# Kernel optimization log

Hardware: AMD Instinct MI355X
Metric: run time of the kernel (lower is better)

## Reference

```python
import jax, jax.numpy as jnp
import numpy as np

B, S, HID = 2, 2048, 1024
H, D = 16, 64
R = 128  # max_relative_position
NREL = 2 * R + 1


def _make_indices():
    i = np.arange(S)[:, None]
    j = np.arange(S)[None, :]
    return np.clip(j - i + R, 0, 2 * R).astype(np.int32)  # [S, S]


def setup_inputs() -> dict:
    key = jax.random.key(0)
    ks = jax.random.split(key, 10)
    sc = 0.02
    return {
        "hidden_states": jax.random.normal(ks[0], (B, S, HID), jnp.float32),
        "st_mask": jnp.ones((B, S), jnp.float32),
        "Wq": jax.random.normal(ks[1], (HID, HID), jnp.float32) * sc,
        "bq": jnp.zeros((HID,), jnp.float32),
        "Wk": jax.random.normal(ks[2], (HID, HID), jnp.float32) * sc,
        "bk": jnp.zeros((HID,), jnp.float32),
        "Wv": jax.random.normal(ks[3], (HID, HID), jnp.float32) * sc,
        "bv": jnp.zeros((HID,), jnp.float32),
        "rel_key_emb": jax.random.normal(ks[4], (NREL, D), jnp.float32) * sc,
        "rel_val_emb": jax.random.normal(ks[5], (NREL, D), jnp.float32) * sc,
        "indices": jnp.asarray(_make_indices()),
    }


def reference(hidden_states, st_mask, Wq, bq, Wk, bk, Wv, bv, rel_key_emb, rel_val_emb, indices):
    b, s, _ = hidden_states.shape

    def heads(x):  # [B,S,HID] -> [B,H,S,D]
        return x.reshape(b, s, H, D).transpose(0, 2, 1, 3)

    q = heads(hidden_states @ Wq.T + bq)
    k = heads(hidden_states @ Wk.T + bk)
    v = heads(hidden_states @ Wv.T + bv)

    scores = jnp.einsum("bhqd,bhkd->bhqk", q, k) / jnp.sqrt(jnp.asarray(D, q.dtype))

    # relative position key bias: gather per (query, key) pair
    rel_scores = jnp.einsum("bhqd,rd->bhqr", q, rel_key_emb)  # [B,H,S,NREL]
    idx = indices[None, None]  # [1,1,S,S]
    scores = scores + jnp.take_along_axis(rel_scores, jnp.broadcast_to(idx, scores.shape), axis=3)

    mask = (1.0 - st_mask) * -10000.0  # [B,S]
    scores = scores + mask[:, None, None, :]

    probs = jax.nn.softmax(scores, axis=-1)  # dropout is identity at eval
    context = jnp.einsum("bhqk,bhkd->bhqd", probs, v)

    # scatter-add probs back onto relative buckets for the value path
    qi = jnp.arange(s)[:, None]  # [S,1] broadcasts with indices [S,S]
    rel_probs = jnp.zeros((b, H, s, NREL), probs.dtype).at[:, :, qi, indices].add(probs)
    context = context + jnp.einsum("bhqr,rd->bhqd", rel_probs, rel_val_emb)

    return context.transpose(0, 2, 1, 3).reshape(b, s, H * D)
```

## Files before the change

### kernel.cpp

```cpp
#include <hip/hip_runtime.h>
#include <math.h>

typedef __bf16 bf16;
typedef __bf16 bf16x8 __attribute__((ext_vector_type(8)));
typedef __bf16 bf16x4 __attribute__((ext_vector_type(4)));
typedef float  f32x4  __attribute__((ext_vector_type(4)));

namespace {
constexpr int B_ = 2, S_ = 2048, HID_ = 1024, H_ = 16, D_ = 64, R_ = 128, NREL_ = 257;
constexpr float LOG2E_ = 1.44269504f;
constexpr float QSC_ = 0.125f * LOG2E_;
}

static __device__ __forceinline__ f32x4 mfma16(bf16x8 a, bf16x8 b, f32x4 c) {
  return __builtin_amdgcn_mfma_f32_16x16x32_bf16(a, b, c, 0, 0, 0);
}
static __device__ __forceinline__ void split2(float f, bf16 &hi, bf16 &lo) {
  hi = (bf16)f; lo = (bf16)(f - (float)hi);
}
static __device__ __forceinline__ float fexp2(float x) {
  return __builtin_amdgcn_exp2f(x);
}
static __device__ __forceinline__ void gload16(const bf16* g, bf16* l) {
  __builtin_amdgcn_global_load_lds(
      (const __attribute__((address_space(1))) void*)g,
      (__attribute__((address_space(3))) void*)l, 16, 0, 0);
}

__global__ __launch_bounds__(256) void prep_kernel(
    const float* __restrict__ st_mask, const float* __restrict__ rkE,
    const float* __restrict__ rvE, const float* __restrict__ hidden,
    const float* __restrict__ Wq, const float* __restrict__ Wk,
    const float* __restrict__ Wv,
    float* __restrict__ msk2, bf16* __restrict__ rkEb, bf16* __restrict__ rvTb,
    bf16* __restrict__ Ahg, bf16* __restrict__ Alg, bf16* __restrict__ Wbg)
{
  const int t0 = blockIdx.x * 256 + threadIdx.x;
  const int NT = gridDim.x * 256;
  for (int t = t0; t < B_ * S_; t += NT)
    msk2[t] = (1.f - st_mask[t]) * -10000.f * LOG2E_;
  for (int t = t0; t < 272 * 64; t += NT) {
    const int bk = t >> 6, d = t & 63;
    rkEb[t] = (bk < NREL_) ? (bf16)(rkE[bk * D_ + d] * 8.0f) : (bf16)0.f;
  }
  for (int t = t0; t < 64 * 288; t += NT) {
    const int d = t / 288, c = t - d * 288;
    rvTb[t] = (c < NREL_) ? (bf16)rvE[c * D_ + d] : (bf16)0.f;
  }
  for (int t = t0; t < (B_ * S_ * HID_) / 4; t += NT) {
    const float4 a = ((const float4*)hidden)[t];
    const float av[4] = {a.x, a.y, a.z, a.w};
    bf16x4 h, o;
#pragma unroll
    for (int i = 0; i < 4; ++i) {
      bf16 th, tl;
      split2(av[i], th, tl);
      h[i] = th; o[i] = tl;
    }
    *(bf16x4*)&Ahg[t * 4] = h;
    *(bf16x4*)&Alg[t * 4] = o;
  }
  for (int t = t0; t < 3 * (HID_ * HID_) / 4; t += NT) {
    const int s = t >> 18, i = t & 262143;
    const float4 wv4 = ((const float4*)(s == 0 ? Wq : s == 1 ? Wk : Wv))[i];
    bf16x4 h;
    h[0] = (bf16)wv4.x; h[1] = (bf16)wv4.y; h[2] = (bf16)wv4.z; h[3] = (bf16)wv4.w;
    *(bf16x4*)&Wbg[s * 1048576 + i * 4] = h;
  }
}

__global__ __launch_bounds__(256, 2) void qkv_mfma_kernel(
    const bf16* __restrict__ Ahg, const bf16* __restrict__ Alg,
    const bf16* __restrict__ Wbg,
    const float* __restrict__ bq, const float* __restrict__ bk,
    const float* __restrict__ bv,
    bf16* __restrict__ Qh, bf16* __restrict__ Ql,
    bf16* __restrict__ Kb, bf16* __restrict__ Vt)
{
  const int swz = ((int)blockIdx.x & 7) * 64 + ((int)blockIdx.x >> 3);
  const int m0 = (swz >> 4) * 128;
  const int n0 = (swz & 15) * 64;
  const int tid = threadIdx.x;
  const int l = tid & 63, w = tid >> 6;
  const int cl = l & 15, g = l >> 4;

  __shared__ __align__(16) bf16 AhS[2][4096];
  __shared__ __align__(16) bf16 AlS[2][4096];
  __shared__ __align__(16) bf16 WS[2][3][2048];

  const int r0 = tid >> 2;
  const int csw = (((tid & 3) ^ (r0 & 3)) << 3);
  const size_t aoff0 = (size_t)(m0 + r0) * HID_ + csw;
  const size_t aoff1 = (size_t)(m0 + 64 + r0) * HID_ + csw;
  const size_t woff  = (size_t)(n0 + r0) * HID_ + csw;
  const int wb = w * 512;

  const int rA0 = w * 16 + cl;
  const int eA0 = rA0 * 32 + 8 * (g ^ (rA0 & 3));
  const int eA1 = eA0 + 2048;
  const int eW  = cl * 32 + 8 * (g ^ (cl & 3));

  f32x4 acc[2][3][4];
#pragma unroll
  for (int hf = 0; hf < 2; ++hf)
#pragma unroll
    for (int s = 0; s < 3; ++s)
#pragma unroll
      for (int nf = 0; nf < 4; ++nf)
#pragma unroll
        for (int i = 0; i < 4; ++i) acc[hf][s][nf][i] = 0.f;

  gload16(Ahg + aoff0, &AhS[0][wb]);
  gload16(Ahg + aoff1, &AhS[0][2048 + wb]);
  gload16(Alg + aoff0, &AlS[0][wb]);
  gload16(Alg + aoff1, &AlS[0][2048 + wb]);
  gload16(Wbg + woff,           &WS[0][0][wb]);
  gload16(Wbg + 1048576 + woff, &WS[0][1][wb]);
  gload16(Wbg + 2097152 + woff, &WS[0][2][wb]);
  __syncthreads();

  int cur = 0;
  for (int kt = 0; kt < HID_ / 32; ++kt) {
    if (kt + 1 < HID_ / 32) {
      const size_t ko = (size_t)(kt + 1) * 32;
      bf16* ah = &AhS[cur ^ 1][0]; bf16* al = &AlS[cur ^ 1][0];
      gload16(Ahg + aoff0 + ko, ah + wb);
      gload16(Ahg + aoff1 + ko, ah + 2048 + wb);
      gload16(Alg + aoff0 + ko, al + wb);
      gload16(Alg + aoff1 + ko, al + 2048 + wb);
      gload16(Wbg + woff + ko,           &WS[cur ^ 1][0][wb]);
      gload16(Wbg + 1048576 + woff + ko, &WS[cur ^ 1][1][wb]);
      gload16(Wbg + 2097152 + woff + ko, &WS[cur ^ 1][2][wb]);
    }

    const bf16x8 fah0 = *(const bf16x8*)&AhS[cur][eA0];
    const bf16x8 fah1 = *(const bf16x8*)&AhS[cur][eA1];
    const bf16x8 fal0 = *(const bf16x8*)&AlS[cur][eA0];
    const bf16x8 fal1 = *(const bf16x8*)&AlS[cur][eA1];
#pragma unroll
    for (int s = 0; s < 3; ++s)
#pragma unroll
      for (int nf = 0; nf < 4; ++nf) {
        const bf16x8 fb = *(const bf16x8*)&WS[cur][s][nf * 512 + eW];
        acc[0][s][nf] = mfma16(fah0, fb, acc[0][s][nf]);
        acc[0][s][nf] = mfma16(fal0, fb, acc[0][s][nf]);
        acc[1][s][nf] = mfma16(fah1, fb, acc[1][s][nf]);
        acc[1][s][nf] = mfma16(fal1, fb, acc[1][s][nf]);
      }
    __syncthreads();
    cur ^= 1;
  }

  const float* bs_[3] = {bq, bk, bv};
#pragma unroll
  for (int s = 0; s < 3; ++s)
#pragma unroll
    for (int nf = 0; nf < 4; ++nf) {
      const int n = n0 + nf * 16 + cl;
      const float bias = bs_[s][n];
      const int hd = n >> 6, d = n & 63;
#pragma unroll
      for (int hf = 0; hf < 2; ++hf)
#pragma unroll
        for (int reg = 0; reg < 4; ++reg) {
          const int m = m0 + hf * 64 + w * 16 + g * 4 + reg;
          const int b = m >> 11, sq = m & (S_ - 1);
          const float val = acc[hf][s][nf][reg] + bias;
          if (s == 0) {
            bf16 h, o; split2(val * QSC_, h, o);
            const size_t idx = ((size_t)(b * H_ + hd) * S_ + sq) * D_ + d;
            Qh[idx] = h; Ql[idx] = o;
          } else if (s == 1) {
            Kb[((size_t)(b * H_ + hd) * S_ + sq) * D_ + d] = (bf16)val;
          } else {
            const int jo = sq & 63;
            const int mc = (jo & 32) | (((jo >> 3) & 1) << 4) | (((jo >> 2) & 1) << 3)
                         | (((jo >> 4) & 1) << 2) | (jo & 3);
            Vt[(((size_t)(b * H_ + hd) * (S_ / 64) + (sq >> 6)) * D_ + d) * 64 + mc]
                = (bf16)val;
          }
        }
    }
}

__global__ __launch_bounds__(512, 4) void attn_kernel(
    const bf16* __restrict__ Qh, const bf16* __restrict__ Ql,
    const bf16* __restrict__ Kb, const bf16* __restrict__ Vt,
    const float* __restrict__ msk2, const bf16* __restrict__ rkEb,
    const bf16* __restrict__ rvTb, float* __restrict__ out)
{
  const int swz = ((int)blockIdx.x & 7) * 128 + ((int)blockIdx.x >> 3);
  const int qt = swz & 31, h = (swz >> 5) & 15, b = swz >> 9;
  const int q0 = qt * 64;
  const int tid = threadIdx.x;
  const int l = tid & 63, w = tid >> 6;
  const int wq = (w & 3) * 16;
  const int wh = w >> 2;
  const int cl = l & 15, g = l >> 4, kg8 = g * 8;
  const int lq = wq + cl;

  __shared__ __align__(16) unsigned char U[36864];
  __shared__ __align__(16) bf16 T[64][288];
  __shared__ float red[2][3][64];
  __shared__ float lsum_s[64];

  bf16* kb0 = (bf16*)&U[0];
  bf16* kb1 = (bf16*)&U[8192];
  bf16* vb0 = (bf16*)&U[16384];
  bf16* vb1 = (bf16*)&U[24576];
  float* ctxredf = (float*)&U[0];

  const size_t bh = (size_t)(b * H_ + h) * S_;
  const bf16* Kbase = Kb + bh * D_;
  const bf16* Vbase = Vt + bh * D_;
  const float* mbase = msk2 + b * S_;

  const int tKr = tid >> 3;
  const int koff = tKr * 64 + (((tid & 7) ^ (tKr & 7)) << 3);

  gload16(Kbase + koff, kb0 + w * 512);
  gload16(Vbase + koff, vb0 + w * 512);

  bf16x8 qh0, qh1, ql0, ql1;
  {
    const size_t base = (bh + q0 + lq) * D_ + kg8;
    qh0 = *(const bf16x8*)(Qh + base);
    qh1 = *(const bf16x8*)(Qh + base + 32);
    ql0 = *(const bf16x8*)(Ql + base);
    ql1 = *(const bf16x8*)(Ql + base + 32);
  }

  {
    const int nt0 = wh ? 9 : 0, ntE = wh ? 17 : 9;
    for (int nt = nt0; nt < ntE; ++nt) {
      f32x4 r; r[0] = r[1] = r[2] = r[3] = 0.f;
      const bf16x8 a0 = *(const bf16x8*)(rkEb + (size_t)(nt * 16 + cl) * 64 + kg8);
      const bf16x8 a1 = *(const bf16x8*)(rkEb + (size_t)(nt * 16 + cl) * 64 + 32 + kg8);
      r = mfma16(a0, qh0, r); r = mfma16(a0, ql0, r);
      r = mfma16(a1, qh1, r); r = mfma16(a1, ql1, r);
      bf16x4 pk;
#pragma unroll
      for (int reg = 0; reg < 4; ++reg) pk[reg] = (bf16)r[reg];
      *(bf16x4*)&T[lq][nt * 16 + g * 4] = pk;
    }
  }
  __syncthreads();

  const float rs_lo = (float)T[lq][0];
  const float rs_hi = (float)T[lq][2 * R_];
  const int qg = q0 + lq;

  f32x4 ctx[4];
#pragma unroll
  for (int nf = 0; nf < 4; ++nf) { ctx[nf][0]=0.f; ctx[nf][1]=0.f; ctx[nf][2]=0.f; ctx[nf][3]=0.f; }
  float lsum = 0.f, plo = 0.f, phi = 0.f;

  const int r00 = wh * 32 + cl, r10 = wh * 32 + 16 + cl;
  const int e00 = r00 * 64 + 8 * (g ^ (r00 & 7)), e01 = r00 * 64 + 8 * ((4 + g) ^ (r00 & 7));
  const int e10 = r10 * 64 + 8 * (g ^ (r10 & 7)), e11 = r10 * 64 + 8 * ((4 + g) ^ (r10 & 7));
  int fv0, fv1, fv2, fv3;
  {
    const int rd0 = 0 * 16 + cl, rd1 = 1 * 16 + cl, rd2 = 2 * 16 + cl, rd3 = 3 * 16 + cl;
    fv0 = rd0 * 64 + 8 * ((4 * wh + g) ^ (rd0 & 7));
    fv1 = rd1 * 64 + 8 * ((4 * wh + g) ^ (rd1 & 7));
    fv2 = rd2 * 64 + 8 * ((4 * wh + g) ^ (rd2 & 7));
    fv3 = rd3 * 64 + 8 * ((4 * wh + g) ^ (rd3 & 7));
  }

  int cur = 0;
  for (int kt = 0; kt < S_ / 64; ++kt) {
    if (kt + 1 < S_ / 64) {
      gload16(Kbase + (size_t)(kt + 1) * 4096 + koff, (cur ? kb0 : kb1) + w * 512);
      gload16(Vbase + (size_t)(kt + 1) * 4096 + koff, (cur ? vb0 : vb1) + w * 512);
    }

    const bf16* kc = cur ? kb1 : kb0;
    const bf16x8 a00 = *(const bf16x8*)&kc[e00];
    const bf16x8 a01 = *(const bf16x8*)&kc[e01];
    const bf16x8 a10 = *(const bf16x8*)&kc[e10];
    const bf16x8 a11 = *(const bf16x8*)&kc[e11];

    f32x4 s0, s1;
    s0[0]=s0[1]=s0[2]=s0[3]=0.f; s1[0]=s1[1]=s1[2]=s1[3]=0.f;
    __builtin_amdgcn_s_setprio(1);
    s0 = mfma16(a00, qh0, s0); s0 = mfma16(a00, ql0, s0);
    s0 = mfma16(a01, qh1, s0); s0 = mfma16(a01, ql1, s0);
    s1 = mfma16(a10, qh0, s1); s1 = mfma16(a10, ql0, s1);
    s1 = mfma16(a11, qh1, s1); s1 = mfma16(a11, ql1, s1);
    __builtin_amdgcn_s_setprio(0);

    const int j0 = kt * 64 + wh * 32;
    const float4 mk0 = *(const float4*)(mbase + j0 + g * 4);
    const float4 mk1 = *(const float4*)(mbase + j0 + 16 + g * 4);
    const int dlt = kt * 64 - q0;
    const int mode = (dlt <= -192) ? 0 : (dlt >= 192 ? 1 : 2);

    bf16x4 pk0, pk1;
#pragma unroll
    for (int nf = 0; nf < 2; ++nf) {
      const f32x4 sa = nf ? s1 : s0;
      const float4 mkv = nf ? mk1 : mk0;
      const float mks[4] = {mkv.x, mkv.y, mkv.z, mkv.w};
      float p[4];
      if (mode == 0) {
#pragma unroll
        for (int reg = 0; reg < 4; ++reg) p[reg] = fexp2(sa[reg] + rs_lo + mks[reg]);
        plo += (p[0] + p[1]) + (p[2] + p[3]);
      } else if (mode == 1) {
#pragma unroll
        for (int reg = 0; reg < 4; ++reg) p[reg] = fexp2(sa[reg] + rs_hi + mks[reg]);
        phi += (p[0] + p[1]) + (p[2] + p[3]);
      } else {
        const int jb = j0 + nf * 16 + g * 4;
#pragma unroll
        for (int reg = 0; reg < 4; ++reg) {
          const int bkv = jb + reg - qg + R_;
          const int bkc = bkv < 0 ? 0 : (bkv > 2 * R_ ? 2 * R_ : bkv);
          const float pv = fexp2(sa[reg] + (float)T[lq][bkc] + mks[reg]);
          p[reg] = pv;
          if (bkv <= 0)           plo += pv;
          else if (bkv >= 2 * R_) phi += pv;
          else                    T[lq][bkv] = (bf16)pv;
        }
      }
      lsum += (p[0] + p[1]) + (p[2] + p[3]);
      bf16x4 pk;
#pragma unroll
      for (int reg = 0; reg < 4; ++reg) pk[reg] = (bf16)p[reg];
      if (nf == 0) pk0 = pk; else pk1 = pk;
    }

    const bf16x8 pa = __builtin_shufflevector(pk0, pk1, 0, 1, 2, 3, 4, 5, 6, 7);
    const bf16* vc = cur ? vb1 : vb0;
    __builtin_amdgcn_s_setprio(1);
    ctx[0] = mfma16(pa, *(const bf16x8*)&vc[fv0], ctx[0]);
    ctx[1] = mfma16(pa, *(const bf16x8*)&vc[fv1], ctx[1]);
    ctx[2] = mfma16(pa, *(const bf16x8*)&vc[fv2], ctx[2]);
    ctx[3] = mfma16(pa, *(const bf16x8*)&vc[fv3], ctx[3]);
    __builtin_amdgcn_s_setprio(0);
    __syncthreads();
    cur ^= 1;
  }

  lsum += __shfl_xor(lsum, 16); lsum += __shfl_xor(lsum, 32);
  plo  += __shfl_xor(plo, 16);  plo  += __shfl_xor(plo, 32);
  phi  += __shfl_xor(phi, 16);  phi  += __shfl_xor(phi, 32);
  if (l < 16) {
    red[wh][0][wq + l] = lsum;
    red[wh][1][wq + l] = plo;
    red[wh][2][wq + l] = phi;
  }
  __syncthreads();

  {
    const int nfs = wh ? 0 : 2;
#pragma unroll
    for (int k2 = 0; k2 < 2; ++k2)
#pragma unroll
      for (int reg = 0; reg < 4; ++reg)
        ctxredf[((wh * 64) + wq + g * 4 + reg) * 36 + k2 * 16 + cl] = ctx[nfs + k2][reg];
  }
  if (tid < 64) {
    lsum_s[tid]    = red[0][0][tid] + red[1][0][tid];
    T[tid][0]      = (bf16)(red[0][1][tid] + red[1][1][tid]);
    T[tid][2 * R_] = (bf16)(red[0][2][tid] + red[1][2][tid]);
  }
  for (int t = tid; t < 64 * 32; t += 512) {
    const int c = t & 31;
    if (c) T[t >> 5][256 + c] = (bf16)0.f;
  }
  if (q0 < R_ || q0 > S_ - R_ - 64) {
    for (int t = tid; t < 64 * 256; t += 512) {
      const int r = t >> 8, c = t & 255;
      if (c >= 1) {
        const int j = q0 + r + c - R_;
        if (j < 0 || j >= S_) T[r][c] = (bf16)0.f;
      }
    }
  }
  __syncthreads();

  const int nfa = wh ? 2 : 0;
  f32x4 cx0 = ctx[nfa], cx1 = ctx[nfa + 1];
#pragma unroll
  for (int reg = 0; reg < 4; ++reg) {
    cx0[reg] += ctxredf[(((wh ^ 1) * 64) + wq + g * 4 + reg) * 36 + cl];
    cx1[reg] += ctxredf[(((wh ^ 1) * 64) + wq + g * 4 + reg) * 36 + 16 + cl];
  }

#pragma unroll
  for (int ks = 0; ks < 9; ++ks) {
    const bf16x8 pa = *(const bf16x8*)&T[lq][ks * 32 + kg8];
    const bf16x8 v0 = *(const bf16x8*)(rvTb + (size_t)(wh * 32 + cl) * 288 + ks * 32 + kg8);
    const bf16x8 v1 = *(const bf16x8*)(rvTb + (size_t)(wh * 32 + 16 + cl) * 288 + ks * 32 + kg8);
    __builtin_amdgcn_s_setprio(1);
    cx0 = mfma16(pa, v0, cx0);
    cx1 = mfma16(pa, v1, cx1);
    __builtin_amdgcn_s_setprio(0);
  }

#pragma unroll
  for (int reg = 0; reg < 4; ++reg) {
    const int qrow = wq + g * 4 + reg;
    const float invl = 1.f / lsum_s[qrow];
    float* op = out + (size_t)(b * S_ + q0 + qrow) * HID_ + h * 64 + wh * 32;
    op[cl]      = cx0[reg] * invl;
    op[16 + cl] = cx1[reg] * invl;
  }
}

extern "C" void kernel_launch(void* const* d_in, const int* in_sizes, int n_in,
                              void* d_out, int out_size, void* d_ws, size_t ws_size,
                              hipStream_t stream)
{
  (void)in_sizes; (void)n_in; (void)out_size; (void)ws_size;
  const float* hidden  = (const float*)d_in[0];
  const float* st_mask = (const float*)d_in[1];
  const float* Wq = (const float*)d_in[2];
  const float* bq = (const float*)d_in[3];
  const float* Wk = (const float*)d_in[4];
  const float* bk = (const float*)d_in[5];
  const float* Wv = (const float*)d_in[6];
  const float* bv = (const float*)d_in[7];
  const float* rkE = (const float*)d_in[8];
  const float* rvE = (const float*)d_in[9];
  float* out = (float*)d_out;

  const size_t per = (size_t)B_ * H_ * S_ * D_;
  char* wsb = (char*)d_ws;
  float* msk2 = (float*)wsb;
  bf16*  rkEb = (bf16*)(wsb + 16384);
  bf16*  rvTb = (bf16*)(wsb + 16384 + 34816);
  char*  base1 = wsb + 16384 + 34816 + 36864;
  bf16* Qh = (bf16*)base1;
  bf16* Ql = Qh + per;
  bf16* Kb = Ql + per;
  bf16* Vt = Kb + per;
  bf16* Ahg = Vt + per;
  bf16* Alg = Ahg + per;
  bf16* Wbg = Alg + per;

  prep_kernel<<<dim3(1024), 256, 0, stream>>>(
      st_mask, rkE, rvE, hidden, Wq, Wk, Wv, msk2, rkEb, rvTb, Ahg, Alg, Wbg);
  qkv_mfma_kernel<<<dim3(512), 256, 0, stream>>>(
      Ahg, Alg, Wbg, bq, bk, bv, Qh, Ql, Kb, Vt);
  attn_kernel<<<dim3(1024), 512, 0, stream>>>(
      Qh, Ql, Kb, Vt, msk2, rkEb, rvTb, out);
}
```

Before: 166.7 us.

## Triple-buffer K tiles, stage mask in LDS, split waits around the barrier

K is now prefetched two tiles ahead using three LDS buffers, while V stays one tile ahead in two buffers. Explicit vmcnt waits plus a raw s_barrier replace the blanket __syncthreads, so PV MFMAs can start before every load has landed. The key mask is converted once to bf16 in LDS instead of being read from global memory every iteration. The last relative bucket (256) is now added as a scalar times rel_val_emb, which shrinks the relative-value MFMA loop from 9 to 8 steps and the T row padding. The hand-written waitcnt counts are fragile, and storing the mask in bf16 introduces small rounding for values other than 0/1.

```diff
diff --git a/kernel.cpp b/kernel.cpp
--- a/kernel.cpp
+++ b/kernel.cpp
@@ -189,6 +189,7 @@
     const float* __restrict__ msk2, const bf16* __restrict__ rkEb,
     const bf16* __restrict__ rvTb, float* __restrict__ out)
 {
+  constexpr int NT = S_ / 64;
   const int swz = ((int)blockIdx.x & 7) * 128 + ((int)blockIdx.x >> 3);
   const int qt = swz & 31, h = (swz >> 5) & 15, b = swz >> 9;
   const int q0 = qt * 64;
@@ -199,15 +200,16 @@
   const int cl = l & 15, g = l >> 4, kg8 = g * 8;
   const int lq = wq + cl;
 
-  __shared__ __align__(16) unsigned char U[36864];
-  __shared__ __align__(16) bf16 T[64][288];
+  __shared__ __align__(16) unsigned char U[40960];
+  __shared__ __align__(16) bf16 T[64][272];
+  __shared__ __align__(16) bf16 msk_l[S_];
   __shared__ float red[2][3][64];
-  __shared__ float lsum_s[64];
-
-  bf16* kb0 = (bf16*)&U[0];
-  bf16* kb1 = (bf16*)&U[8192];
-  bf16* vb0 = (bf16*)&U[16384];
-  bf16* vb1 = (bf16*)&U[24576];
+
+  bf16* kA = (bf16*)&U[0];
+  bf16* kB = (bf16*)&U[8192];
+  bf16* kC = (bf16*)&U[16384];
+  bf16* vA = (bf16*)&U[24576];
+  bf16* vB = (bf16*)&U[32768];
   float* ctxredf = (float*)&U[0];
 
   const size_t bh = (size_t)(b * H_ + h) * S_;
@@ -218,8 +220,16 @@
   const int tKr = tid >> 3;
   const int koff = tKr * 64 + (((tid & 7) ^ (tKr & 7)) << 3);
 
-  gload16(Kbase + koff, kb0 + w * 512);
-  gload16(Vbase + koff, vb0 + w * 512);
+  gload16(Kbase + koff,        kA + w * 512);
+  gload16(Kbase + 4096 + koff, kB + w * 512);
+  gload16(Vbase + koff,        vA + w * 512);
+
+  {
+    const float4 m4 = *(const float4*)(mbase + tid * 4);
+    bf16x4 mb;
+    mb[0] = (bf16)m4.x; mb[1] = (bf16)m4.y; mb[2] = (bf16)m4.z; mb[3] = (bf16)m4.w;
+    *(bf16x4*)&msk_l[tid * 4] = mb;
+  }
 
   bf16x8 qh0, qh1, ql0, ql1;
   {
@@ -260,25 +270,24 @@
   const int e10 = r10 * 64 + 8 * (g ^ (r10 & 7)), e11 = r10 * 64 + 8 * ((4 + g) ^ (r10 & 7));
   int fv0, fv1, fv2, fv3;
   {
-    const int rd0 = 0 * 16 + cl, rd1 = 1 * 16 + cl, rd2 = 2 * 16 + cl, rd3 = 3 * 16 + cl;
+    const int rd0 = cl, rd1 = 16 + cl, rd2 = 32 + cl, rd3 = 48 + cl;
     fv0 = rd0 * 64 + 8 * ((4 * wh + g) ^ (rd0 & 7));
     fv1 = rd1 * 64 + 8 * ((4 * wh + g) ^ (rd1 & 7));
     fv2 = rd2 * 64 + 8 * ((4 * wh + g) ^ (rd2 & 7));
     fv3 = rd3 * 64 + 8 * ((4 * wh + g) ^ (rd3 & 7));
   }
 
-  int cur = 0;
-  for (int kt = 0; kt < S_ / 64; ++kt) {
-    if (kt + 1 < S_ / 64) {
-      gload16(Kbase + (size_t)(kt + 1) * 4096 + koff, (cur ? kb0 : kb1) + w * 512);
-      gload16(Vbase + (size_t)(kt + 1) * 4096 + koff, (cur ? vb0 : vb1) + w * 512);
-    }
-
-    const bf16* kc = cur ? kb1 : kb0;
-    const bf16x8 a00 = *(const bf16x8*)&kc[e00];
-    const bf16x8 a01 = *(const bf16x8*)&kc[e01];
-    const bf16x8 a10 = *(const bf16x8*)&kc[e10];
-    const bf16x8 a11 = *(const bf16x8*)&kc[e11];
+  bf16* kR = kA; bf16* kM = kB; bf16* kW = kC;
+  bf16* vR = vA; bf16* vW = vB;
+
+  for (int kt = 0; kt < NT; ++kt) {
+    if (kt + 2 < NT) gload16(Kbase + (size_t)(kt + 2) * 4096 + koff, kW + w * 512);
+    if (kt + 1 < NT) gload16(Vbase + (size_t)(kt + 1) * 4096 + koff, vW + w * 512);
+
+    const bf16x8 a00 = *(const bf16x8*)&kR[e00];
+    const bf16x8 a01 = *(const bf16x8*)&kR[e01];
+    const bf16x8 a10 = *(const bf16x8*)&kR[e10];
+    const bf16x8 a11 = *(const bf16x8*)&kR[e11];
 
     f32x4 s0, s1;
     s0[0]=s0[1]=s0[2]=s0[3]=0.f; s1[0]=s1[1]=s1[2]=s1[3]=0.f;
@@ -290,8 +299,8 @@
     __builtin_amdgcn_s_setprio(0);
 
     const int j0 = kt * 64 + wh * 32;
-    const float4 mk0 = *(const float4*)(mbase + j0 + g * 4);
-    const float4 mk1 = *(const float4*)(mbase + j0 + 16 + g * 4);
+    const bf16x4 mb0 = *(const bf16x4*)&msk_l[j0 + g * 4];
+    const bf16x4 mb1 = *(const bf16x4*)&msk_l[j0 + 16 + g * 4];
     const int dlt = kt * 64 - q0;
     const int mode = (dlt <= -192) ? 0 : (dlt >= 192 ? 1 : 2);
 
@@ -299,8 +308,10 @@
 #pragma unroll
     for (int nf = 0; nf < 2; ++nf) {
       const f32x4 sa = nf ? s1 : s0;
-      const float4 mkv = nf ? mk1 : mk0;
-      const float mks[4] = {mkv.x, mkv.y, mkv.z, mkv.w};
+      const bf16x4 mkv = nf ? mb1 : mb0;
+      float mks[4];
+#pragma unroll
+      for (int i = 0; i < 4; ++i) mks[i] = (float)mkv[i];
       float p[4];
       if (mode == 0) {
 #pragma unroll
@@ -330,16 +341,27 @@
       if (nf == 0) pk0 = pk; else pk1 = pk;
     }
 
+    if (kt < NT - 2)      asm volatile("s_waitcnt vmcnt(2)" ::: "memory");
+    else if (kt == NT - 2) asm volatile("s_waitcnt vmcnt(1)" ::: "memory");
+    else                  asm volatile("s_waitcnt vmcnt(0)" ::: "memory");
+    __builtin_amdgcn_sched_barrier(0);
+
     const bf16x8 pa = __builtin_shufflevector(pk0, pk1, 0, 1, 2, 3, 4, 5, 6, 7);
-    const bf16* vc = cur ? vb1 : vb0;
     __builtin_amdgcn_s_setprio(1);
-    ctx[0] = mfma16(pa, *(const bf16x8*)&vc[fv0], ctx[0]);
-    ctx[1] = mfma16(pa, *(const bf16x8*)&vc[fv1], ctx[1]);
-    ctx[2] = mfma16(pa, *(const bf16x8*)&vc[fv2], ctx[2]);
-    ctx[3] = mfma16(pa, *(const bf16x8*)&vc[fv3], ctx[3]);
+    ctx[0] = mfma16(pa, *(const bf16x8*)&vR[fv0], ctx[0]);
+    ctx[1] = mfma16(pa, *(const bf16x8*)&vR[fv1], ctx[1]);
+    ctx[2] = mfma16(pa, *(const bf16x8*)&vR[fv2], ctx[2]);
+    ctx[3] = mfma16(pa, *(const bf16x8*)&vR[fv3], ctx[3]);
     __builtin_amdgcn_s_setprio(0);
-    __syncthreads();
-    cur ^= 1;
+
+    if (kt < NT - 2) asm volatile("s_waitcnt vmcnt(1)" ::: "memory");
+    else             asm volatile("s_waitcnt vmcnt(0)" ::: "memory");
+    __builtin_amdgcn_sched_barrier(0);
+    __builtin_amdgcn_s_barrier();
+    __builtin_amdgcn_sched_barrier(0);
+
+    bf16* t0 = kR; kR = kM; kM = kW; kW = t0;
+    bf16* t1 = vR; vR = vW; vW = t1;
   }
 
   lsum += __shfl_xor(lsum, 16); lsum += __shfl_xor(lsum, 32);
@@ -361,13 +383,9 @@
         ctxredf[((wh * 64) + wq + g * 4 + reg) * 36 + k2 * 16 + cl] = ctx[nfs + k2][reg];
   }
   if (tid < 64) {
-    lsum_s[tid]    = red[0][0][tid] + red[1][0][tid];
-    T[tid][0]      = (bf16)(red[0][1][tid] + red[1][1][tid]);
-    T[tid][2 * R_] = (bf16)(red[0][2][tid] + red[1][2][tid]);
-  }
-  for (int t = tid; t < 64 * 32; t += 512) {
-    const int c = t & 31;
-    if (c) T[t >> 5][256 + c] = (bf16)0.f;
+    red[0][0][tid] += red[1][0][tid];
+    T[tid][0] = (bf16)(red[0][1][tid] + red[1][1][tid]);
+    red[0][2][tid] += red[1][2][tid];
   }
   if (q0 < R_ || q0 > S_ - R_ - 64) {
     for (int t = tid; t < 64 * 256; t += 512) {
@@ -389,7 +407,7 @@
   }
 
 #pragma unroll
-  for (int ks = 0; ks < 9; ++ks) {
+  for (int ks = 0; ks < 8; ++ks) {
     const bf16x8 pa = *(const bf16x8*)&T[lq][ks * 32 + kg8];
     const bf16x8 v0 = *(const bf16x8*)(rvTb + (size_t)(wh * 32 + cl) * 288 + ks * 32 + kg8);
     const bf16x8 v1 = *(const bf16x8*)(rvTb + (size_t)(wh * 32 + 16 + cl) * 288 + ks * 32 + kg8);
@@ -398,14 +416,17 @@
     cx1 = mfma16(pa, v1, cx1);
     __builtin_amdgcn_s_setprio(0);
   }
+  const float rv256a = (float)rvTb[(size_t)(wh * 32 + cl) * 288 + 256];
+  const float rv256b = (float)rvTb[(size_t)(wh * 32 + 16 + cl) * 288 + 256];
 
 #pragma unroll
   for (int reg = 0; reg < 4; ++reg) {
     const int qrow = wq + g * 4 + reg;
-    const float invl = 1.f / lsum_s[qrow];
+    const float invl = 1.f / red[0][0][qrow];
+    const float phq  = red[0][2][qrow];
     float* op = out + (size_t)(b * S_ + q0 + qrow) * HID_ + h * 64 + wh * 32;
-    op[cl]      = cx0[reg] * invl;
-    op[16 + cl] = cx1[reg] * invl;
+    op[cl]      = (cx0[reg] + phq * rv256a) * invl;
+    op[16 + cl] = (cx1[reg] + phq * rv256b) * invl;
   }
 }
 
```

Result: faster. 160.0 us (-4.0%).
